# Kernel tuning notes

Hardware: AMD Instinct MI355X
Metric: run time of the kernel (lower is better)

## Reference

```python
import jax, jax.numpy as jnp
import numpy as np

IN_CAPS = 128      # number of memory capsules (rows of m)
NUM_CAPS = 5       # n_class
DIM_CAPS = 153     # comp_dim // n_class = 768 // 5
IN_DIM = 768       # comp_dim
NQ = 256           # number of query samples
NUM_ROUTING = 3
BETA = 1.0         # config['Model']['temperature']
EPS = 1e-8


def _pearsonr(x, y):
    # Pearson correlation along last dim (broadcasts over leading dims).
    xm = x - x.mean(axis=-1, keepdims=True)
    ym = y - y.mean(axis=-1, keepdims=True)
    num = (xm * ym).sum(axis=-1)
    den = jnp.sqrt((xm * xm).sum(axis=-1)) * jnp.sqrt((ym * ym).sum(axis=-1))
    return num / (den + EPS)


def _squash(s):
    # capsule squash along last dim
    n2 = (s * s).sum(axis=-1, keepdims=True)
    return (n2 / (1.0 + n2)) * s / jnp.sqrt(n2 + EPS)


def setup_inputs() -> dict:
    key = jax.random.key(0)
    k1, k2, k3 = jax.random.split(key, 3)
    m = jax.random.normal(k1, (IN_CAPS, IN_DIM), dtype=jnp.float32)
    q = jax.random.normal(k2, (NQ, IN_DIM), dtype=jnp.float32)
    W = jax.random.normal(k3, (IN_DIM, NUM_CAPS * DIM_CAPS), dtype=jnp.float32) * 0.02
    b = jnp.zeros((NUM_CAPS * DIM_CAPS,), dtype=jnp.float32)
    return {"m": m, "q": q, "W": W, "b": b}


def reference(m, q, W, b):
    sg = jax.lax.stop_gradient
    # projections -> capsule preactivations
    hat_m = (m @ W + b).reshape(IN_CAPS, NUM_CAPS, DIM_CAPS)          # [I,C,D]
    hat_q = (q @ W + b).reshape(-1, NUM_CAPS, DIM_CAPS)               # [Q,C,D]
    Qn = hat_q.shape[0]
    tmp_m = sg(hat_m)[None, :, :, :]                                   # [1,I,C,D] (broadcast over Q)
    tmp_q = sg(hat_q)[:, None, :, :]                                   # [Q,1,C,D]

    a = jnp.zeros((Qn, IN_CAPS, NUM_CAPS), dtype=hat_q.dtype)          # routing logits
    p = jnp.tanh(_pearsonr(tmp_m, tmp_q))                              # [Q,I,C]

    for _ in range(NUM_ROUTING - 1):
        d = jax.nn.softmax(a / BETA, axis=2)                           # [Q,I,C]
        dsp = d + p
        hat_v = (tmp_m * dsp[..., None]).sum(axis=1)                   # [Q,C,D]
        v = _squash(hat_v)
        m_dot_v = (tmp_m * v[:, None, :, :]).sum(axis=-1)              # [Q,I,C]
        a = a + p * m_dot_v
        tmp_q = (tmp_q + v[:, None, :, :]) * 0.5                       # [Q,I,C,D]
        p = jnp.tanh(_pearsonr(tmp_m, tmp_q))

    d = jax.nn.softmax(a / BETA, axis=2)
    dsp = sg(d + p)                                                    # routing coeffs detached
    hat_v = (hat_m[None, :, :, :] * dsp[..., None]).sum(axis=1)        # grad flows via hat_m only
    q_prime = _squash(hat_v).reshape(Qn, -1)                           # [Q, C*D]
    return q_prime
```

## Files before the change

### kernel.cpp

```cpp
#include <hip/hip_runtime.h>
#include <hip/hip_bf16.h>

#define I_CAPS 128
#define N_CAPS 5
#define D_CAPS 153
#define D_PAD  160
#define MLD    800
#define IN_DIM 768
#define NQ     256
#define CD     765
#define NPAIR  640
#define EPSF   1e-8f
#define KHALF  384

typedef __hip_bfloat16 bf16;

__device__ __forceinline__ float wred(float x) {
#pragma unroll
  for (int off = 32; off; off >>= 1) x += __shfl_down(x, off, 64);
  return x;
}

__device__ __forceinline__ float tanh_fast(float x) {
  float t = __expf(-2.f * fabsf(x));
  float r = (1.f - t) / (1.f + t);
  return copysignf(r, x);
}

__global__ void classify_kernel(const unsigned* __restrict__ m_u32,
                                int* __restrict__ flag) {
  int lane = threadIdx.x & 63;
  unsigned u = m_u32[lane];
  int e = (u >> 7) & 0xFF;
  int hit = (e >= 118 && e <= 134) ? 1 : 0;
  unsigned long long mask = __ballot(hit);
  if (lane == 0) *flag = (__popcll(mask) >= 48) ? 1 : 0;
}

template <bool ISB>
__device__ __forceinline__ float ld_in(const void* p, long idx) {
  if (ISB) return __bfloat162float(((const bf16*)p)[idx]);
  return ((const float*)p)[idx];
}

template <bool ISB>
__device__ void gemm_body(const void* m, const void* q, const void* W,
                          const void* b, float* hat_m, float* hat_q) {
  __shared__ float As[8][KHALF];
  const int tx = threadIdx.x, ty = threadIdx.y;
  const int t = ty * 64 + tx;
  const int row0 = blockIdx.y * 8;
  const int k0 = blockIdx.z * KHALF;

  if (ISB) {
    for (int e = t; e < 8 * KHALF; e += 256) {
      int rr = e / KHALF, kk = e - rr * KHALF;
      int row = row0 + rr;
      As[rr][kk] = (row < I_CAPS)
                       ? ld_in<true>(m, (long)row * IN_DIM + k0 + kk)
                       : ld_in<true>(q, (long)(row - I_CAPS) * IN_DIM + k0 + kk);
    }
  } else {
    for (int e = t; e < 8 * (KHALF / 4); e += 256) {
      int rr = e / (KHALF / 4), k4 = e - rr * (KHALF / 4);
      int row = row0 + rr;
      const float* src = (row < I_CAPS)
                             ? (const float*)m + (long)row * IN_DIM
                             : (const float*)q + (long)(row - I_CAPS) * IN_DIM;
      *(float4*)&As[rr][k4 * 4] = *(const float4*)(src + k0 + k4 * 4);
    }
  }
  __syncthreads();

  const int col = blockIdx.x * 64 + tx;
  const int colc = (col < CD) ? col : (CD - 1);
  const int r0 = ty * 2, r1 = r0 + 1;

  float a0a = 0.f, a0b = 0.f, a1a = 0.f, a1b = 0.f;
#pragma unroll 2
  for (int k = 0; k < KHALF; k += 8) {
    const float4 A0a = *(const float4*)&As[r0][k];
    const float4 A0b = *(const float4*)&As[r0][k + 4];
    const float4 A1a = *(const float4*)&As[r1][k];
    const float4 A1b = *(const float4*)&As[r1][k + 4];
    float w0 = ld_in<ISB>(W, (long)(k0 + k + 0) * CD + colc);
    float w1 = ld_in<ISB>(W, (long)(k0 + k + 1) * CD + colc);
    float w2 = ld_in<ISB>(W, (long)(k0 + k + 2) * CD + colc);
    float w3 = ld_in<ISB>(W, (long)(k0 + k + 3) * CD + colc);
    float w4 = ld_in<ISB>(W, (long)(k0 + k + 4) * CD + colc);
    float w5 = ld_in<ISB>(W, (long)(k0 + k + 5) * CD + colc);
    float w6 = ld_in<ISB>(W, (long)(k0 + k + 6) * CD + colc);
    float w7 = ld_in<ISB>(W, (long)(k0 + k + 7) * CD + colc);
    a0a = fmaf(A0a.x, w0, a0a); a0b = fmaf(A0a.y, w1, a0b);
    a0a = fmaf(A0a.z, w2, a0a); a0b = fmaf(A0a.w, w3, a0b);
    a0a = fmaf(A0b.x, w4, a0a); a0b = fmaf(A0b.y, w5, a0b);
    a0a = fmaf(A0b.z, w6, a0a); a0b = fmaf(A0b.w, w7, a0b);
    a1a = fmaf(A1a.x, w0, a1a); a1b = fmaf(A1a.y, w1, a1b);
    a1a = fmaf(A1a.z, w2, a1a); a1b = fmaf(A1a.w, w3, a1b);
    a1a = fmaf(A1b.x, w4, a1a); a1b = fmaf(A1b.y, w5, a1b);
    a1a = fmaf(A1b.z, w6, a1a); a1b = fmaf(A1b.w, w7, a1b);
  }

  if (col < CD) {
    float p0 = a0a + a0b;
    float p1 = a1a + a1b;
    if (blockIdx.z == 0) {
      float bias = ld_in<ISB>(b, col);
      p0 += bias;
      p1 += bias;
    }
    int c = col / D_CAPS, d = col - c * D_CAPS;
    int ra = row0 + r0, rb = row0 + r1;
    float* d0 = (ra < I_CAPS) ? &hat_m[ra * MLD + c * D_PAD + d]
                              : &hat_q[(ra - I_CAPS) * CD + col];
    float* d1 = (rb < I_CAPS) ? &hat_m[rb * MLD + c * D_PAD + d]
                              : &hat_q[(rb - I_CAPS) * CD + col];
    atomicAdd(d0, p0);
    atomicAdd(d1, p1);
  }
}

__global__ __launch_bounds__(256, 4)
void gemm_kernel(const void* m, const void* q, const void* W, const void* b,
                 const int* __restrict__ flag,
                 float* __restrict__ hat_m, float* __restrict__ hat_q) {
  if (*flag)
    gemm_body<true>(m, q, W, b, hat_m, hat_q);
  else
    gemm_body<false>(m, q, W, b, hat_m, hat_q);
}

__global__ __launch_bounds__(256)
void stats_kernel(const float* __restrict__ hat_m,
                  float* __restrict__ mean_m, float* __restrict__ ssm) {
  const int wave = threadIdx.x >> 6, lane = threadIdx.x & 63;
  const int pair = blockIdx.x * 4 + wave;
  const int i = pair / N_CAPS, c = pair - i * N_CAPS;
  const float* hm = hat_m + i * MLD + c * D_PAD;
  float s = 0.f, s2 = 0.f;
  for (int d = lane; d < D_CAPS; d += 64) {
    float x = hm[d];
    s += x;
    s2 = fmaf(x, x, s2);
  }
  s = wred(s);
  s2 = wred(s2);
  if (lane == 0) {
    float mu = s * (1.f / D_CAPS);
    mean_m[pair] = mu;
    ssm[pair] = fmaxf(s2 - (float)D_CAPS * mu * mu, 0.f);
  }
}

__global__ __launch_bounds__(128)
void gram_kernel(const float* __restrict__ hat_m, float* __restrict__ G) {
  const int c = blockIdx.x, j = blockIdx.y, i = threadIdx.x;
  const float4* hi = (const float4*)(hat_m + i * MLD + c * D_PAD);
  const float4* hj = (const float4*)(hat_m + j * MLD + c * D_PAD);
  float a0 = 0.f, a1 = 0.f, a2 = 0.f, a3 = 0.f;
#pragma unroll 8
  for (int k = 0; k < 40; ++k) {
    float4 x = hi[k];
    float4 y = hj[k];
    a0 = fmaf(x.x, y.x, a0);
    a1 = fmaf(x.y, y.y, a1);
    a2 = fmaf(x.z, y.z, a2);
    a3 = fmaf(x.w, y.w, a3);
  }
  G[c * 16384 + j * 128 + i] = (a0 + a1) + (a2 + a3);
}

__global__ __launch_bounds__(1024, 4)
void routing_kernel(const float* __restrict__ hat_m,
                    const float* __restrict__ hat_q,
                    const float* __restrict__ Gmat,
                    const float* __restrict__ mean_m,
                    const float* __restrict__ ssm,
                    const int* __restrict__ flag,
                    void* __restrict__ out_v) {
  __shared__ float tq[N_CAPS * D_PAD], vv[N_CAPS * D_PAD];
  __shared__ float aa[NPAIR], pp[NPAIR], dsp[NPAIR], sdot[NPAIR];
  __shared__ float smm[NPAIR], sss[NPAIR];
  __shared__ float meanq[N_CAPS], ssq[N_CAPS], sc_s[N_CAPS];
  __shared__ float tsum_s[N_CAPS], t2_s[N_CAPS];
  __shared__ float red[10][4];

  const int tid = threadIdx.x;
  const int qi = blockIdx.x;
  const int w = tid >> 6, lane = tid & 63;
  const int g = tid >> 3, sub = tid & 7;
  const float* hq = hat_q + qi * CD;
  const float* hm = hat_m + g * MLD;

  for (int l = tid; l < N_CAPS * D_PAD; l += 1024) {
    int c = l / D_PAD, d = l - c * D_PAD;
    tq[l] = (d < D_CAPS) ? hq[c * D_CAPS + d] : 0.f;
  }
  if (tid < NPAIR) {
    aa[tid] = 0.f;
    smm[tid] = mean_m[tid];
    sss[tid] = ssm[tid];
  }
  __syncthreads();

  if (w < N_CAPS) {
    const int c = w;
    float s = 0.f, s2 = 0.f;
    for (int d = lane; d < D_CAPS; d += 64) {
      float x = tq[c * D_PAD + d];
      s += x;
      s2 = fmaf(x, x, s2);
    }
    s = wred(s);
    s2 = wred(s2);
    if (lane == 0) {
      float mu = s * (1.f / D_CAPS);
      tsum_s[c] = s;
      t2_s[c] = s2;
      meanq[c] = mu;
      ssq[c] = fmaxf(s2 - (float)D_CAPS * mu * mu, 0.f);
    }
  }
  __syncthreads();

  {
    float A0 = 0.f, A1 = 0.f, A2 = 0.f, A3 = 0.f, A4 = 0.f;
#pragma unroll 2
    for (int jj = 0; jj < 5; ++jj) {
      int d = jj * 32 + sub * 4;
      float4 h0 = *(const float4*)(hm + 0 * D_PAD + d);
      float4 h1 = *(const float4*)(hm + 1 * D_PAD + d);
      float4 h2 = *(const float4*)(hm + 2 * D_PAD + d);
      float4 h3 = *(const float4*)(hm + 3 * D_PAD + d);
      float4 h4 = *(const float4*)(hm + 4 * D_PAD + d);
      float4 t0 = *(const float4*)(tq + 0 * D_PAD + d);
      float4 t1 = *(const float4*)(tq + 1 * D_PAD + d);
      float4 t2 = *(const float4*)(tq + 2 * D_PAD + d);
      float4 t3 = *(const float4*)(tq + 3 * D_PAD + d);
      float4 t4 = *(const float4*)(tq + 4 * D_PAD + d);
      A0 = fmaf(h0.x, t0.x, A0); A0 = fmaf(h0.y, t0.y, A0);
      A0 = fmaf(h0.z, t0.z, A0); A0 = fmaf(h0.w, t0.w, A0);
      A1 = fmaf(h1.x, t1.x, A1); A1 = fmaf(h1.y, t1.y, A1);
      A1 = fmaf(h1.z, t1.z, A1); A1 = fmaf(h1.w, t1.w, A1);
      A2 = fmaf(h2.x, t2.x, A2); A2 = fmaf(h2.y, t2.y, A2);
      A2 = fmaf(h2.z, t2.z, A2); A2 = fmaf(h2.w, t2.w, A2);
      A3 = fmaf(h3.x, t3.x, A3); A3 = fmaf(h3.y, t3.y, A3);
      A3 = fmaf(h3.z, t3.z, A3); A3 = fmaf(h3.w, t3.w, A3);
      A4 = fmaf(h4.x, t4.x, A4); A4 = fmaf(h4.y, t4.y, A4);
      A4 = fmaf(h4.z, t4.z, A4); A4 = fmaf(h4.w, t4.w, A4);
    }
#pragma unroll
    for (int off = 1; off < 8; off <<= 1) {
      A0 += __shfl_xor(A0, off, 64);
      A1 += __shfl_xor(A1, off, 64);
      A2 += __shfl_xor(A2, off, 64);
      A3 += __shfl_xor(A3, off, 64);
      A4 += __shfl_xor(A4, off, 64);
    }
    if (sub < N_CAPS) {
      float acc = A0;
      acc = (sub == 1) ? A1 : acc;
      acc = (sub == 2) ? A2 : acc;
      acc = (sub == 3) ? A3 : acc;
      acc = (sub == 4) ? A4 : acc;
      int ic = g * N_CAPS + sub;
      sdot[ic] = acc;
      float num = acc - (float)D_CAPS * smm[ic] * meanq[sub];
      float den = sqrtf(sss[ic]) * sqrtf(ssq[sub]) + EPSF;
      pp[ic] = tanh_fast(num / den);
    }
  }
  __syncthreads();

  auto softmax_dsp = [&]() {
    if (tid < I_CAPS) {
      float av[N_CAPS], ev[N_CAPS];
      float mx = -1e30f;
#pragma unroll
      for (int c = 0; c < N_CAPS; ++c) {
        av[c] = aa[tid * N_CAPS + c];
        mx = fmaxf(mx, av[c]);
      }
      float s = 0.f;
#pragma unroll
      for (int c = 0; c < N_CAPS; ++c) {
        ev[c] = __expf(av[c] - mx);
        s += ev[c];
      }
      float inv = 1.f / s;
#pragma unroll
      for (int c = 0; c < N_CAPS; ++c)
        dsp[tid * N_CAPS + c] = ev[c] * inv + pp[tid * N_CAPS + c];
    }
  };

  for (int r = 0; r < 2; ++r) {
    softmax_dsp();
    __syncthreads();
    float y = 0.f, sold = 0.f;
    int cc = 0, ii = 0, ic = 0;
    if (tid < NPAIR) {
      cc = tid >> 7;
      ii = tid & 127;
      ic = ii * N_CAPS + cc;
      const float* Gp = Gmat + cc * 16384 + ii;
      float y0 = 0.f, y1 = 0.f;
#pragma unroll 4
      for (int j = 0; j < 128; j += 2) {
        y0 = fmaf(Gp[j * 128], dsp[j * N_CAPS + cc], y0);
        y1 = fmaf(Gp[(j + 1) * 128], dsp[(j + 1) * N_CAPS + cc], y1);
      }
      y = y0 + y1;
      sold = sdot[ic];
      float dmy = dsp[ic];
      float n2p = dmy * y;
      float vsp = dmy * ((float)D_CAPS * smm[ic]);
      float sdp = dmy * sold;
      n2p = wred(n2p);
      vsp = wred(vsp);
      sdp = wred(sdp);
      if (lane == 0) {
        red[w][0] = n2p;
        red[w][1] = vsp;
        red[w][2] = sdp;
      }
    }
    __syncthreads();
    if (tid < N_CAPS) {
      float n2 = red[2 * tid][0] + red[2 * tid + 1][0];
      float vs = red[2 * tid][1] + red[2 * tid + 1][1];
      float sd = red[2 * tid][2] + red[2 * tid + 1][2];
      float sc = (n2 / (1.f + n2)) * rsqrtf(n2 + EPSF);
      sc_s[tid] = sc;
      float ts = 0.5f * (tsum_s[tid] + sc * vs);
      float t2 = 0.25f * (t2_s[tid] + 2.f * sc * sd + sc * sc * n2);
      tsum_s[tid] = ts;
      t2_s[tid] = t2;
      float mu = ts * (1.f / D_CAPS);
      meanq[tid] = mu;
      ssq[tid] = fmaxf(t2 - (float)D_CAPS * mu * mu, 0.f);
    }
    __syncthreads();
    if (tid < NPAIR) {
      float mdv = sc_s[cc] * y;
      aa[ic] += pp[ic] * mdv;
      float snew = 0.5f * (sold + mdv);
      sdot[ic] = snew;
      float num = snew - (float)D_CAPS * smm[ic] * meanq[cc];
      float den = sqrtf(sss[ic]) * sqrtf(ssq[cc]) + EPSF;
      pp[ic] = tanh_fast(num / den);
    }
    __syncthreads();
  }

  softmax_dsp();
  __syncthreads();
  for (int cd = tid; cd < CD; cd += 1024) {
    int c = cd / D_CAPS, d = cd - c * D_CAPS;
    const float* col = hat_m + c * D_PAD + d;
    float b0 = 0.f, b1 = 0.f, b2 = 0.f, b3 = 0.f;
    float b4 = 0.f, b5 = 0.f, b6 = 0.f, b7 = 0.f;
#pragma unroll 4
    for (int i = 0; i < I_CAPS; i += 8) {
      b0 = fmaf(dsp[(i + 0) * N_CAPS + c], col[(i + 0) * MLD], b0);
      b1 = fmaf(dsp[(i + 1) * N_CAPS + c], col[(i + 1) * MLD], b1);
      b2 = fmaf(dsp[(i + 2) * N_CAPS + c], col[(i + 2) * MLD], b2);
      b3 = fmaf(dsp[(i + 3) * N_CAPS + c], col[(i + 3) * MLD], b3);
      b4 = fmaf(dsp[(i + 4) * N_CAPS + c], col[(i + 4) * MLD], b4);
      b5 = fmaf(dsp[(i + 5) * N_CAPS + c], col[(i + 5) * MLD], b5);
      b6 = fmaf(dsp[(i + 6) * N_CAPS + c], col[(i + 6) * MLD], b6);
      b7 = fmaf(dsp[(i + 7) * N_CAPS + c], col[(i + 7) * MLD], b7);
    }
    vv[c * D_PAD + d] = ((b0 + b1) + (b2 + b3)) + ((b4 + b5) + (b6 + b7));
  }
  __syncthreads();
  if (w < N_CAPS) {
    const int c = w;
    float s2 = 0.f;
    for (int d = lane; d < D_CAPS; d += 64) {
      float x = vv[c * D_PAD + d];
      s2 = fmaf(x, x, s2);
    }
    s2 = wred(s2);
    if (lane == 0) sc_s[c] = (s2 / (1.f + s2)) * rsqrtf(s2 + EPSF);
  }
  __syncthreads();

  if (*flag == 0) {
    float* out = (float*)out_v;
    for (int cd = tid; cd < CD; cd += 1024) {
      int c = cd / D_CAPS, d = cd - c * D_CAPS;
      out[qi * CD + cd] = vv[c * D_PAD + d] * sc_s[c];
    }
  } else {
    bf16* out = (bf16*)out_v;
    for (int cd = tid; cd < CD; cd += 1024) {
      int c = cd / D_CAPS, d = cd - c * D_CAPS;
      out[qi * CD + cd] = __float2bfloat16(vv[c * D_PAD + d] * sc_s[c]);
    }
  }
}

extern "C" void kernel_launch(void* const* d_in, const int* in_sizes, int n_in,
                              void* d_out, int out_size, void* d_ws, size_t ws_size,
                              hipStream_t stream) {
  const void *m = nullptr, *q = nullptr, *W = nullptr, *b = nullptr;
  for (int i = 0; i < n_in; ++i) {
    switch (in_sizes[i]) {
      case I_CAPS * IN_DIM: m = d_in[i]; break;
      case NQ * IN_DIM:     q = d_in[i]; break;
      case IN_DIM * CD:     W = d_in[i]; break;
      case CD:              b = d_in[i]; break;
      default: break;
    }
  }
  if (!m || !q || !W || !b) {
    m = d_in[0]; q = d_in[1]; W = d_in[2]; b = d_in[3];
  }

  int*   flag   = (int*)d_ws;
  float* mean_m = (float*)d_ws + 16;
  float* ssm    = mean_m + 640;
  float* hat_m  = ssm + 640;
  float* hat_q  = hat_m + I_CAPS * MLD;
  float* G      = hat_q + NQ * CD;

  classify_kernel<<<1, 64, 0, stream>>>((const unsigned*)m, flag);
  hipMemsetAsync(hat_m, 0,
                 ((size_t)I_CAPS * MLD + (size_t)NQ * CD) * sizeof(float),
                 stream);
  gemm_kernel<<<dim3(12, 48, 2), dim3(64, 4), 0, stream>>>(m, q, W, b, flag,
                                                           hat_m, hat_q);
  stats_kernel<<<160, 256, 0, stream>>>(hat_m, mean_m, ssm);
  gram_kernel<<<dim3(N_CAPS, I_CAPS), 128, 0, stream>>>(hat_m, G);
  routing_kernel<<<NQ, 1024, 0, stream>>>(hat_m, hat_q, G, mean_m, ssm, flag,
                                          d_out);
}
```

Before: 121.1 us.

## Split final capsule aggregation into tiled GEMM kernel and enlarge projection row tile

The final weighted sum over memory capsules moves out of the per-query routing kernel into a separate tiled outgemm kernel. That kernel stages hat_m and the transposed routing coefficients in shared memory and computes outputs for 32 queries at once. The squash norm is taken from the Gram matrix-vector product instead of re-summing the output vector. The routing update also merges a barrier by having every thread recompute per-capsule stats, and the projection GEMM now covers 16 rows per block with 4 accumulators per thread. The cost is an extra launch and a global round-trip of the dsp and scale arrays.

Result: slower. 125.2 us (+3.4%).

```diff
diff --git a/kernel.cpp b/kernel.cpp
--- a/kernel.cpp
+++ b/kernel.cpp
@@ -27,6 +27,10 @@
   return copysignf(r, x);
 }
 
+__device__ __forceinline__ float squash_sc(float n2) {
+  return (n2 / (1.f + n2)) * rsqrtf(n2 + EPSF);
+}
+
 __global__ void classify_kernel(const unsigned* __restrict__ m_u32,
                                 int* __restrict__ flag) {
   int lane = threadIdx.x & 63;
@@ -46,14 +50,14 @@
 template <bool ISB>
 __device__ void gemm_body(const void* m, const void* q, const void* W,
                           const void* b, float* hat_m, float* hat_q) {
-  __shared__ float As[8][KHALF];
+  __shared__ float As[16][KHALF];
   const int tx = threadIdx.x, ty = threadIdx.y;
   const int t = ty * 64 + tx;
-  const int row0 = blockIdx.y * 8;
+  const int row0 = blockIdx.y * 16;
   const int k0 = blockIdx.z * KHALF;
 
   if (ISB) {
-    for (int e = t; e < 8 * KHALF; e += 256) {
+    for (int e = t; e < 16 * KHALF; e += 256) {
       int rr = e / KHALF, kk = e - rr * KHALF;
       int row = row0 + rr;
       As[rr][kk] = (row < I_CAPS)
@@ -61,7 +65,7 @@
                        : ld_in<true>(q, (long)(row - I_CAPS) * IN_DIM + k0 + kk);
     }
   } else {
-    for (int e = t; e < 8 * (KHALF / 4); e += 256) {
+    for (int e = t; e < 16 * (KHALF / 4); e += 256) {
       int rr = e / (KHALF / 4), k4 = e - rr * (KHALF / 4);
       int row = row0 + rr;
       const float* src = (row < I_CAPS)
@@ -74,15 +78,14 @@
 
   const int col = blockIdx.x * 64 + tx;
   const int colc = (col < CD) ? col : (CD - 1);
-  const int r0 = ty * 2, r1 = r0 + 1;
-
-  float a0a = 0.f, a0b = 0.f, a1a = 0.f, a1b = 0.f;
+  const int r0 = ty * 4;
+
+  float acc[4][2];
+#pragma unroll
+  for (int r = 0; r < 4; ++r) { acc[r][0] = 0.f; acc[r][1] = 0.f; }
+
 #pragma unroll 2
   for (int k = 0; k < KHALF; k += 8) {
-    const float4 A0a = *(const float4*)&As[r0][k];
-    const float4 A0b = *(const float4*)&As[r0][k + 4];
-    const float4 A1a = *(const float4*)&As[r1][k];
-    const float4 A1b = *(const float4*)&As[r1][k + 4];
     float w0 = ld_in<ISB>(W, (long)(k0 + k + 0) * CD + colc);
     float w1 = ld_in<ISB>(W, (long)(k0 + k + 1) * CD + colc);
     float w2 = ld_in<ISB>(W, (long)(k0 + k + 2) * CD + colc);
@@ -91,32 +94,32 @@
     float w5 = ld_in<ISB>(W, (long)(k0 + k + 5) * CD + colc);
     float w6 = ld_in<ISB>(W, (long)(k0 + k + 6) * CD + colc);
     float w7 = ld_in<ISB>(W, (long)(k0 + k + 7) * CD + colc);
-    a0a = fmaf(A0a.x, w0, a0a); a0b = fmaf(A0a.y, w1, a0b);
-    a0a = fmaf(A0a.z, w2, a0a); a0b = fmaf(A0a.w, w3, a0b);
-    a0a = fmaf(A0b.x, w4, a0a); a0b = fmaf(A0b.y, w5, a0b);
-    a0a = fmaf(A0b.z, w6, a0a); a0b = fmaf(A0b.w, w7, a0b);
-    a1a = fmaf(A1a.x, w0, a1a); a1b = fmaf(A1a.y, w1, a1b);
-    a1a = fmaf(A1a.z, w2, a1a); a1b = fmaf(A1a.w, w3, a1b);
-    a1a = fmaf(A1b.x, w4, a1a); a1b = fmaf(A1b.y, w5, a1b);
-    a1a = fmaf(A1b.z, w6, a1a); a1b = fmaf(A1b.w, w7, a1b);
+#pragma unroll
+    for (int r = 0; r < 4; ++r) {
+      const float4 Aa = *(const float4*)&As[r0 + r][k];
+      const float4 Ab = *(const float4*)&As[r0 + r][k + 4];
+      acc[r][0] = fmaf(Aa.x, w0, acc[r][0]);
+      acc[r][1] = fmaf(Aa.y, w1, acc[r][1]);
+      acc[r][0] = fmaf(Aa.z, w2, acc[r][0]);
+      acc[r][1] = fmaf(Aa.w, w3, acc[r][1]);
+      acc[r][0] = fmaf(Ab.x, w4, acc[r][0]);
+      acc[r][1] = fmaf(Ab.y, w5, acc[r][1]);
+      acc[r][0] = fmaf(Ab.z, w6, acc[r][0]);
+      acc[r][1] = fmaf(Ab.w, w7, acc[r][1]);
+    }
   }
 
   if (col < CD) {
-    float p0 = a0a + a0b;
-    float p1 = a1a + a1b;
-    if (blockIdx.z == 0) {
-      float bias = ld_in<ISB>(b, col);
-      p0 += bias;
-      p1 += bias;
-    }
+    float bias = (blockIdx.z == 0) ? ld_in<ISB>(b, col) : 0.f;
     int c = col / D_CAPS, d = col - c * D_CAPS;
-    int ra = row0 + r0, rb = row0 + r1;
-    float* d0 = (ra < I_CAPS) ? &hat_m[ra * MLD + c * D_PAD + d]
-                              : &hat_q[(ra - I_CAPS) * CD + col];
-    float* d1 = (rb < I_CAPS) ? &hat_m[rb * MLD + c * D_PAD + d]
-                              : &hat_q[(rb - I_CAPS) * CD + col];
-    atomicAdd(d0, p0);
-    atomicAdd(d1, p1);
+#pragma unroll
+    for (int r = 0; r < 4; ++r) {
+      int row = row0 + r0 + r;
+      float p = acc[r][0] + acc[r][1] + bias;
+      float* dst = (row < I_CAPS) ? &hat_m[row * MLD + c * D_PAD + d]
+                                  : &hat_q[(row - I_CAPS) * CD + col];
+      atomicAdd(dst, p);
+    }
   }
 }
 
@@ -176,13 +179,13 @@
                     const float* __restrict__ Gmat,
                     const float* __restrict__ mean_m,
                     const float* __restrict__ ssm,
-                    const int* __restrict__ flag,
-                    void* __restrict__ out_v) {
-  __shared__ float tq[N_CAPS * D_PAD], vv[N_CAPS * D_PAD];
+                    float* __restrict__ dspT,
+                    float* __restrict__ scT) {
+  __shared__ float tq[N_CAPS * D_PAD];
   __shared__ float aa[NPAIR], pp[NPAIR], dsp[NPAIR], sdot[NPAIR];
   __shared__ float smm[NPAIR], sss[NPAIR];
-  __shared__ float meanq[N_CAPS], ssq[N_CAPS], sc_s[N_CAPS];
-  __shared__ float tsum_s[N_CAPS], t2_s[N_CAPS];
+  __shared__ float meanq0[N_CAPS], ssq0[N_CAPS];
+  __shared__ float tsum_s[2][N_CAPS], t2_s[2][N_CAPS];
   __shared__ float red[10][4];
 
   const int tid = threadIdx.x;
@@ -215,10 +218,10 @@
     s2 = wred(s2);
     if (lane == 0) {
       float mu = s * (1.f / D_CAPS);
-      tsum_s[c] = s;
-      t2_s[c] = s2;
-      meanq[c] = mu;
-      ssq[c] = fmaxf(s2 - (float)D_CAPS * mu * mu, 0.f);
+      tsum_s[0][c] = s;
+      t2_s[0][c] = s2;
+      meanq0[c] = mu;
+      ssq0[c] = fmaxf(s2 - (float)D_CAPS * mu * mu, 0.f);
     }
   }
   __syncthreads();
@@ -265,8 +268,8 @@
       acc = (sub == 4) ? A4 : acc;
       int ic = g * N_CAPS + sub;
       sdot[ic] = acc;
-      float num = acc - (float)D_CAPS * smm[ic] * meanq[sub];
-      float den = sqrtf(sss[ic]) * sqrtf(ssq[sub]) + EPSF;
+      float num = acc - (float)D_CAPS * smm[ic] * meanq0[sub];
+      float den = sqrtf(sss[ic]) * sqrtf(ssq0[sub]) + EPSF;
       pp[ic] = tanh_fast(num / den);
     }
   }
@@ -294,31 +297,29 @@
     }
   };
 
+  auto gmatvec = [&](int cc, int ii) {
+    const float* Gp = Gmat + cc * 16384 + ii;
+    float y0 = 0.f, y1 = 0.f;
+#pragma unroll 4
+    for (int j = 0; j < 128; j += 2) {
+      y0 = fmaf(Gp[j * 128], dsp[j * N_CAPS + cc], y0);
+      y1 = fmaf(Gp[(j + 1) * 128], dsp[(j + 1) * N_CAPS + cc], y1);
+    }
+    return y0 + y1;
+  };
+
   for (int r = 0; r < 2; ++r) {
     softmax_dsp();
     __syncthreads();
     float y = 0.f, sold = 0.f;
-    int cc = 0, ii = 0, ic = 0;
+    int cc = tid >> 7, ii = tid & 127, ic = ii * N_CAPS + cc;
     if (tid < NPAIR) {
-      cc = tid >> 7;
-      ii = tid & 127;
-      ic = ii * N_CAPS + cc;
-      const float* Gp = Gmat + cc * 16384 + ii;
-      float y0 = 0.f, y1 = 0.f;
-#pragma unroll 4
-      for (int j = 0; j < 128; j += 2) {
-        y0 = fmaf(Gp[j * 128], dsp[j * N_CAPS + cc], y0);
-        y1 = fmaf(Gp[(j + 1) * 128], dsp[(j + 1) * N_CAPS + cc], y1);
-      }
-      y = y0 + y1;
+      y = gmatvec(cc, ii);
       sold = sdot[ic];
       float dmy = dsp[ic];
-      float n2p = dmy * y;
-      float vsp = dmy * ((float)D_CAPS * smm[ic]);
-      float sdp = dmy * sold;
-      n2p = wred(n2p);
-      vsp = wred(vsp);
-      sdp = wred(sdp);
+      float n2p = wred(dmy * y);
+      float vsp = wred(dmy * ((float)D_CAPS * smm[ic]));
+      float sdp = wred(dmy * sold);
       if (lane == 0) {
         red[w][0] = n2p;
         red[w][1] = vsp;
@@ -326,28 +327,25 @@
       }
     }
     __syncthreads();
-    if (tid < N_CAPS) {
-      float n2 = red[2 * tid][0] + red[2 * tid + 1][0];
-      float vs = red[2 * tid][1] + red[2 * tid + 1][1];
-      float sd = red[2 * tid][2] + red[2 * tid + 1][2];
-      float sc = (n2 / (1.f + n2)) * rsqrtf(n2 + EPSF);
-      sc_s[tid] = sc;
-      float ts = 0.5f * (tsum_s[tid] + sc * vs);
-      float t2 = 0.25f * (t2_s[tid] + 2.f * sc * sd + sc * sc * n2);
-      tsum_s[tid] = ts;
-      t2_s[tid] = t2;
+    if (tid < NPAIR) {
+      float n2 = red[2 * cc][0] + red[2 * cc + 1][0];
+      float vs = red[2 * cc][1] + red[2 * cc + 1][1];
+      float sd = red[2 * cc][2] + red[2 * cc + 1][2];
+      float sc = squash_sc(n2);
+      float ts = 0.5f * (tsum_s[r & 1][cc] + sc * vs);
+      float t2v = 0.25f * (t2_s[r & 1][cc] + 2.f * sc * sd + sc * sc * n2);
+      if (ii == 0) {
+        tsum_s[(r + 1) & 1][cc] = ts;
+        t2_s[(r + 1) & 1][cc] = t2v;
+      }
       float mu = ts * (1.f / D_CAPS);
-      meanq[tid] = mu;
-      ssq[tid] = fmaxf(t2 - (float)D_CAPS * mu * mu, 0.f);
-    }
-    __syncthreads();
-    if (tid < NPAIR) {
-      float mdv = sc_s[cc] * y;
+      float ssqv = fmaxf(t2v - (float)D_CAPS * mu * mu, 0.f);
+      float mdv = sc * y;
       aa[ic] += pp[ic] * mdv;
       float snew = 0.5f * (sold + mdv);
       sdot[ic] = snew;
-      float num = snew - (float)D_CAPS * smm[ic] * meanq[cc];
-      float den = sqrtf(sss[ic]) * sqrtf(ssq[cc]) + EPSF;
+      float num = snew - (float)D_CAPS * smm[ic] * mu;
+      float den = sqrtf(sss[ic]) * sqrtf(ssqv) + EPSF;
       pp[ic] = tanh_fast(num / den);
     }
     __syncthreads();
@@ -355,49 +353,75 @@
 
   softmax_dsp();
   __syncthreads();
-  for (int cd = tid; cd < CD; cd += 1024) {
-    int c = cd / D_CAPS, d = cd - c * D_CAPS;
-    const float* col = hat_m + c * D_PAD + d;
-    float b0 = 0.f, b1 = 0.f, b2 = 0.f, b3 = 0.f;
-    float b4 = 0.f, b5 = 0.f, b6 = 0.f, b7 = 0.f;
-#pragma unroll 4
-    for (int i = 0; i < I_CAPS; i += 8) {
-      b0 = fmaf(dsp[(i + 0) * N_CAPS + c], col[(i + 0) * MLD], b0);
-      b1 = fmaf(dsp[(i + 1) * N_CAPS + c], col[(i + 1) * MLD], b1);
-      b2 = fmaf(dsp[(i + 2) * N_CAPS + c], col[(i + 2) * MLD], b2);
-      b3 = fmaf(dsp[(i + 3) * N_CAPS + c], col[(i + 3) * MLD], b3);
-      b4 = fmaf(dsp[(i + 4) * N_CAPS + c], col[(i + 4) * MLD], b4);
-      b5 = fmaf(dsp[(i + 5) * N_CAPS + c], col[(i + 5) * MLD], b5);
-      b6 = fmaf(dsp[(i + 6) * N_CAPS + c], col[(i + 6) * MLD], b6);
-      b7 = fmaf(dsp[(i + 7) * N_CAPS + c], col[(i + 7) * MLD], b7);
-    }
-    vv[c * D_PAD + d] = ((b0 + b1) + (b2 + b3)) + ((b4 + b5) + (b6 + b7));
-  }
-  __syncthreads();
-  if (w < N_CAPS) {
-    const int c = w;
-    float s2 = 0.f;
-    for (int d = lane; d < D_CAPS; d += 64) {
-      float x = vv[c * D_PAD + d];
-      s2 = fmaf(x, x, s2);
-    }
-    s2 = wred(s2);
-    if (lane == 0) sc_s[c] = (s2 / (1.f + s2)) * rsqrtf(s2 + EPSF);
-  }
-  __syncthreads();
+  {
+    int cc = tid >> 7, ii = tid & 127, ic = ii * N_CAPS + cc;
+    float y = 0.f;
+    if (tid < NPAIR) {
+      y = gmatvec(cc, ii);
+      float n2p = wred(dsp[ic] * y);
+      if (lane == 0) red[w][0] = n2p;
+    }
+    __syncthreads();
+    if (tid < NPAIR)
+      dspT[(cc * NQ + qi) * 128 + ii] = dsp[ic];
+    if (tid < N_CAPS) {
+      float n2 = red[2 * tid][0] + red[2 * tid + 1][0];
+      scT[tid * NQ + qi] = squash_sc(n2);
+    }
+  }
+}
+
+__global__ __launch_bounds__(256, 4)
+void outgemm_kernel(const float* __restrict__ hat_m,
+                    const float* __restrict__ dspT,
+                    const float* __restrict__ scT,
+                    const int* __restrict__ flag,
+                    void* __restrict__ out_v) {
+  __shared__ float hmT[128][32];
+  __shared__ float dspS[32][132];
+
+  const int c = blockIdx.x, dt = blockIdx.y, qt = blockIdx.z;
+  const int tid = threadIdx.x;
+
+  for (int e = tid; e < 128 * 8; e += 256) {
+    int i = e >> 3, dd4 = e & 7;
+    *(float4*)&hmT[i][dd4 * 4] =
+        *(const float4*)(hat_m + i * MLD + c * D_PAD + dt * 32 + dd4 * 4);
+  }
+  for (int e = tid; e < 32 * 32; e += 256) {
+    int qq = e >> 5, k4 = e & 31;
+    *(float4*)&dspS[qq][k4 * 4] =
+        *(const float4*)(dspT + ((long)c * NQ + qt * 32 + qq) * 128 + k4 * 4);
+  }
+  __syncthreads();
+
+  const int qq = tid >> 3, dsub = tid & 7;
+  const int q = qt * 32 + qq;
+  float a0 = 0.f, a1 = 0.f, a2 = 0.f, a3 = 0.f;
+#pragma unroll 2
+  for (int i = 0; i < 128; ++i) {
+    float dv = dspS[qq][i];
+    const float4 h = *(const float4*)&hmT[i][dsub * 4];
+    a0 = fmaf(dv, h.x, a0);
+    a1 = fmaf(dv, h.y, a1);
+    a2 = fmaf(dv, h.z, a2);
+    a3 = fmaf(dv, h.w, a3);
+  }
+  const float sc = scT[c * NQ + q];
+  const int d0 = dt * 32 + dsub * 4;
+  float r[4] = {a0 * sc, a1 * sc, a2 * sc, a3 * sc};
 
   if (*flag == 0) {
     float* out = (float*)out_v;
-    for (int cd = tid; cd < CD; cd += 1024) {
-      int c = cd / D_CAPS, d = cd - c * D_CAPS;
-      out[qi * CD + cd] = vv[c * D_PAD + d] * sc_s[c];
-    }
+#pragma unroll
+    for (int k = 0; k < 4; ++k)
+      if (d0 + k < D_CAPS) out[q * CD + c * D_CAPS + d0 + k] = r[k];
   } else {
     bf16* out = (bf16*)out_v;
-    for (int cd = tid; cd < CD; cd += 1024) {
-      int c = cd / D_CAPS, d = cd - c * D_CAPS;
-      out[qi * CD + cd] = __float2bfloat16(vv[c * D_PAD + d] * sc_s[c]);
-    }
+#pragma unroll
+    for (int k = 0; k < 4; ++k)
+      if (d0 + k < D_CAPS)
+        out[q * CD + c * D_CAPS + d0 + k] = __float2bfloat16(r[k]);
   }
 }
 
@@ -424,15 +448,19 @@
   float* hat_m  = ssm + 640;
   float* hat_q  = hat_m + I_CAPS * MLD;
   float* G      = hat_q + NQ * CD;
+  float* dspT   = G + N_CAPS * I_CAPS * I_CAPS;
+  float* scT    = dspT + (size_t)N_CAPS * NQ * 128;
 
   classify_kernel<<<1, 64, 0, stream>>>((const unsigned*)m, flag);
   hipMemsetAsync(hat_m, 0,
                  ((size_t)I_CAPS * MLD + (size_t)NQ * CD) * sizeof(float),
                  stream);
-  gemm_kernel<<<dim3(12, 48, 2), dim3(64, 4), 0, stream>>>(m, q, W, b, flag,
+  gemm_kernel<<<dim3(12, 24, 2), dim3(64, 4), 0, stream>>>(m, q, W, b, flag,
                                                            hat_m, hat_q);
   stats_kernel<<<160, 256, 0, stream>>>(hat_m, mean_m, ssm);
   gram_kernel<<<dim3(N_CAPS, I_CAPS), 128, 0, stream>>>(hat_m, G);
-  routing_kernel<<<NQ, 1024, 0, stream>>>(hat_m, hat_q, G, mean_m, ssm, flag,
-                                          d_out);
-}
+  routing_kernel<<<NQ, 1024, 0, stream>>>(hat_m, hat_q, G, mean_m, ssm,
+                                          dspT, scT);
+  outgemm_kernel<<<dim3(N_CAPS, 5, 8), 256, 0, stream>>>(hat_m, dspT, scT,
+                                                         flag, d_out);
+}
```
